# Kernel optimization log

Hardware: AMD Instinct MI355X
Metric: run time of the kernel (lower is better)

Reference implementation:

```python
import jax, jax.numpy as jnp
import numpy as np
import math

B, QL, KL, D = 8, 2048, 2048, 1024


def setup_inputs() -> dict:
    key = jax.random.key(0)
    ks = jax.random.split(key, 9)
    s = 1.0 / math.sqrt(D)
    return {
        "q_embd": jax.random.normal(ks[0], (B, QL, D), jnp.float32),
        "k_embd": jax.random.normal(ks[1], (B, KL, D), jnp.float32),
        "v_embd": jax.random.normal(ks[2], (B, KL, D), jnp.float32),
        "Wq": jax.random.normal(ks[3], (D, D), jnp.float32) * s,
        "bq": jax.random.normal(ks[4], (D,), jnp.float32) * s,
        "Wk": jax.random.normal(ks[5], (D, D), jnp.float32) * s,
        "bk": jax.random.normal(ks[6], (D,), jnp.float32) * s,
        "Wv": jax.random.normal(ks[7], (D, D), jnp.float32) * s,
        "bv": jax.random.normal(ks[8], (D,), jnp.float32) * s,
    }


def reference(q_embd, k_embd, v_embd, Wq, bq, Wk, bk, Wv, bv):
    # Linear projections (torch Linear: x @ W^T + b); head_size==1 so
    # the permute/view multi-head reshuffle is an identity.
    q = jnp.einsum("bsd,hd->bsh", q_embd, Wq) + bq  # [B,QL,D]
    k = jnp.einsum("bsd,hd->bsh", k_embd, Wk) + bk  # [B,KL,D]
    v = jnp.einsum("bsd,hd->bsh", v_embd, Wv) + bv  # [B,KL,D]
    # scaled_dot score: [B,QL,KL]
    scale = 1.0 / jnp.sqrt(jnp.asarray(q.shape[-1], q.dtype))
    score = jnp.einsum("bqd,bkd->bqk", q, k) * scale
    attn = jax.nn.softmax(score, axis=-1)
    out = jnp.einsum("bqk,bkd->bqd", attn, v)  # [B,QL,D]
    return out
```

## Files before the change

kernel.cpp:

```cpp
#include <hip/hip_runtime.h>
#include <hip/hip_bf16.h>

typedef float f32x4 __attribute__((ext_vector_type(4)));
typedef __bf16 bf16x8 __attribute__((ext_vector_type(8)));
typedef unsigned short u16x4 __attribute__((ext_vector_type(4)));

__device__ __forceinline__ unsigned short f2bf(float f) {
  unsigned u = __builtin_bit_cast(unsigned, f);
  u += 0x7FFFu + ((u >> 16) & 1u);
  return (unsigned short)(u >> 16);
}
__device__ __forceinline__ float bf2f(unsigned short h) {
  unsigned u = ((unsigned)h) << 16;
  return __builtin_bit_cast(float, u);
}

__device__ __forceinline__ void gload_lds16(const void* g, void* l) {
  __builtin_amdgcn_global_load_lds(
      (const __attribute__((address_space(1))) void*)g,
      (__attribute__((address_space(3))) void*)l, 16, 0, 0);
}

constexpr int BM = 256, BN = 256, BK = 64;

#define BAR() __builtin_amdgcn_s_barrier()
#define VMW(N) asm volatile("s_waitcnt vmcnt(" #N ")" ::: "memory")
#define PRIO(x) __builtin_amdgcn_s_setprio(x)

#define MM(a_, b_, c_)                                                        \
  c_ = __builtin_amdgcn_mfma_f32_16x16x32_bf16(                               \
      __builtin_bit_cast(bf16x8, a_), __builtin_bit_cast(bf16x8, b_), c_, 0, 0, 0)

template <int OUT_MODE, bool HAS_BIAS>
__global__ __launch_bounds__(512, 2) void gemm256(
    const unsigned short* __restrict__ A, const unsigned short* __restrict__ B,
    const float* __restrict__ bias, float scale, void* __restrict__ Cv,
    int N, int K, long sA, long sB, long sC, const float* __restrict__ rsum,
    int gx, int gy) {
  __shared__ char sm[131072];

  const int nwg = gridDim.x;
  int id = blockIdx.x;
  id = (id & 7) * (nwg >> 3) + (id >> 3);
  const int bx = id % gx;
  const int by = (id / gx) % gy;
  const int bz = id / (gx * gy);

  const int t = threadIdx.x;
  const int lane = t & 63;
  const int w = t >> 6;
  const int wm = w >> 2;
  const int wn = w & 3;

  const int rowBase = by * BM;
  const int colBase = bx * BN;
  const unsigned short* Ab = A + sA * bz;
  const unsigned short* Bb = B + sB * bz;
  const int NT = K >> 6;

  const int srl = lane >> 3;
  const int schunk = (lane & 7) ^ srl;

#define STAGE_A(tt, h, d)                                                     \
  do {                                                                        \
    int _kt = (tt); if (_kt > NT - 1) _kt = NT - 1;                           \
    const int _k0 = _kt << 6;                                                 \
    _Pragma("unroll") for (int _j = 0; _j < 2; ++_j) {                        \
      const int _r = (w + 8 * _j) * 8 + srl;                                  \
      gload_lds16(Ab + (size_t)(rowBase + (h) * 128 + _r) * K + _k0 + schunk * 8, \
                  sm + (d) * 32768 + (h) * 16384 + (w + 8 * _j) * 1024);      \
    }                                                                         \
  } while (0)
#define STAGE_B(tt, h, d)                                                     \
  do {                                                                        \
    int _kt = (tt); if (_kt > NT - 1) _kt = NT - 1;                           \
    const int _k0 = _kt << 6;                                                 \
    _Pragma("unroll") for (int _j = 0; _j < 2; ++_j) {                        \
      const int _r = (w + 8 * _j) * 8 + srl;                                  \
      gload_lds16(Bb + (size_t)(colBase + (h) * 128 + _r) * K + _k0 + schunk * 8, \
                  sm + 65536 + (d) * 32768 + (h) * 16384 + (w + 8 * _j) * 1024); \
    }                                                                         \
  } while (0)

  const int lr = lane & 15;
  const int g0 = lane >> 4;
  const int sw0 = (g0 ^ (lr & 7)) << 4;
  const int sw1 = ((g0 + 4) ^ (lr & 7)) << 4;
  const int aBase = wm * 8192 + lr * 128;
  const int bBase = 65536 + wn * 4096 + lr * 128;

  uint4 Ar[4][2], Br0[2][2], Br1[2][2];
  f32x4 acc[8][4];
#pragma unroll
  for (int m = 0; m < 8; ++m)
#pragma unroll
    for (int n = 0; n < 4; ++n) acc[m][n] = (f32x4){0.f, 0.f, 0.f, 0.f};

#define READ_A(d, mh)                                                         \
  do {                                                                        \
    _Pragma("unroll") for (int f = 0; f < 4; ++f) {                           \
      Ar[f][0] = *(const uint4*)(sm + (d) * 32768 + (mh) * 16384 + aBase + f * 2048 + sw0); \
      Ar[f][1] = *(const uint4*)(sm + (d) * 32768 + (mh) * 16384 + aBase + f * 2048 + sw1); \
    }                                                                         \
  } while (0)
#define READ_B0(d)                                                            \
  do {                                                                        \
    _Pragma("unroll") for (int f = 0; f < 2; ++f) {                           \
      Br0[f][0] = *(const uint4*)(sm + (d) * 32768 + bBase + f * 2048 + sw0); \
      Br0[f][1] = *(const uint4*)(sm + (d) * 32768 + bBase + f * 2048 + sw1); \
    }                                                                         \
  } while (0)
#define READ_B1(d)                                                            \
  do {                                                                        \
    _Pragma("unroll") for (int f = 0; f < 2; ++f) {                           \
      Br1[f][0] = *(const uint4*)(sm + (d) * 32768 + 16384 + bBase + f * 2048 + sw0); \
      Br1[f][1] = *(const uint4*)(sm + (d) * 32768 + 16384 + bBase + f * 2048 + sw1); \
    }                                                                         \
  } while (0)

#define MFMA_Q(Bset, mh, nh)                                                  \
  do {                                                                        \
    _Pragma("unroll") for (int kk = 0; kk < 2; ++kk)                          \
        _Pragma("unroll") for (int mf = 0; mf < 4; ++mf)                      \
            _Pragma("unroll") for (int nf = 0; nf < 2; ++nf)                  \
                MM(Ar[mf][kk], Bset[nf][kk], acc[(mh) * 4 + mf][(nh) * 2 + nf]); \
  } while (0)

#define TILE2(t_, d_)                                                         \
  do {                                                                        \
     READ_B0(d_); READ_B1(d_); READ_A(d_, 0);                       \
    STAGE_A((t_) + 1, 1, (d_) ^ 1);                                           \
    BAR();                                                                    \
    PRIO(1); MFMA_Q(Br0, 0, 0); MFMA_Q(Br1, 0, 1); PRIO(0);                   \
    BAR();                                                                    \
     READ_A(d_, 1);                                                 \
    STAGE_A((t_) + 2, 0, d_); STAGE_B((t_) + 2, 0, d_); STAGE_B((t_) + 2, 1, d_); \
    BAR();                                                                    \
    PRIO(1); MFMA_Q(Br1, 1, 1); MFMA_Q(Br0, 1, 0); PRIO(0);                   \
    VMW(6);                                                                   \
    BAR();                                                                    \
  } while (0)

  STAGE_A(0, 0, 0); STAGE_B(0, 0, 0); STAGE_B(0, 1, 0); STAGE_A(0, 1, 0);
  STAGE_A(1, 0, 1); STAGE_B(1, 0, 1); STAGE_B(1, 1, 1);
  VMW(6);
  BAR();

  for (int i = 0; i < (NT >> 1); ++i) {
    TILE2(2 * i, 0);
    TILE2(2 * i + 1, 1);
  }
  VMW(0);

#pragma unroll
  for (int n = 0; n < 4; ++n) {
    const int col = colBase + (n >> 1) * 128 + wn * 32 + (n & 1) * 16 + lr;
    float bvv = 0.f;
    if constexpr (HAS_BIAS) bvv = bias[col];
#pragma unroll
    for (int m = 0; m < 8; ++m) {
      const int row0 = rowBase + (m >> 2) * 128 + wm * 64 + (m & 3) * 16 + g0 * 4;
      f32x4 v = acc[m][n];
      if constexpr (OUT_MODE == 0) {
        unsigned short* C = (unsigned short*)Cv + sC * bz;
#pragma unroll
        for (int r = 0; r < 4; ++r)
          C[(size_t)(row0 + r) * N + col] = f2bf(v[r] * scale + bvv);
      } else if constexpr (OUT_MODE == 1) {
        unsigned short* C = (unsigned short*)Cv;
        const int b = row0 >> 11, s = row0 & 2047;
        u16x4 pk;
#pragma unroll
        for (int r = 0; r < 4; ++r) pk[r] = f2bf(v[r] * scale + bvv);
        *(u16x4*)&C[((size_t)b * N + col) * 2048 + s] = pk;
      } else if constexpr (OUT_MODE == 2) {
        float* C = (float*)Cv + sC * bz;
        const float4 lv = *(const float4*)&rsum[(size_t)bz * 2048 + row0];
        C[(size_t)(row0 + 0) * N + col] = v[0] / lv.x;
        C[(size_t)(row0 + 1) * N + col] = v[1] / lv.y;
        C[(size_t)(row0 + 2) * N + col] = v[2] / lv.z;
        C[(size_t)(row0 + 3) * N + col] = v[3] / lv.w;
      } else {
        unsigned short* C = (unsigned short*)Cv + sC * bz;
#pragma unroll
        for (int r = 0; r < 4; ++r)
          C[(size_t)(row0 + r) * N + col] = f2bf(__expf(v[r] * scale));
      }
    }
  }
}

__global__ __launch_bounds__(256) void conv_pair(
    const float* __restrict__ e, const float* __restrict__ wt,
    unsigned short* __restrict__ eo, unsigned short* __restrict__ wo,
    int ne8, int nw8) {
  const int tot = ne8 + nw8;
  const int stride = gridDim.x * 256;
  for (int i = blockIdx.x * 256 + threadIdx.x; i < tot; i += stride) {
    const float* src;
    unsigned short* dst;
    int k;
    if (i < ne8) { src = e; dst = eo; k = i; }
    else { src = wt; dst = wo; k = i - ne8; }
    float4 a = ((const float4*)src)[2 * k];
    float4 b = ((const float4*)src)[2 * k + 1];
    unsigned short h[8];
    h[0] = f2bf(a.x); h[1] = f2bf(a.y); h[2] = f2bf(a.z); h[3] = f2bf(a.w);
    h[4] = f2bf(b.x); h[5] = f2bf(b.y); h[6] = f2bf(b.z); h[7] = f2bf(b.w);
    ((uint4*)dst)[k] = *(uint4*)h;
  }
}

__global__ __launch_bounds__(256) void rowsum_kernel(
    const unsigned short* __restrict__ E, float* __restrict__ out) {
  const size_t row = blockIdx.x;
  const unsigned short* p = E + row * 2048;
  const int t = threadIdx.x;
  const int lane = t & 63, wid = t >> 6;

  uint4 x = ((const uint4*)p)[t];
  const unsigned short* hs = (const unsigned short*)&x;
  float s = 0.f;
#pragma unroll
  for (int j = 0; j < 8; ++j) s += bf2f(hs[j]);
#pragma unroll
  for (int d = 1; d < 64; d <<= 1) s += __shfl_xor(s, d);
  __shared__ float red[4];
  if (lane == 0) red[wid] = s;
  __syncthreads();
  if (t == 0) out[row] = red[0] + red[1] + red[2] + red[3];
}

extern "C" void kernel_launch(void* const* d_in, const int* in_sizes, int n_in,
                              void* d_out, int out_size, void* d_ws, size_t ws_size,
                              hipStream_t stream) {
  const float* q_embd = (const float*)d_in[0];
  const float* k_embd = (const float*)d_in[1];
  const float* v_embd = (const float*)d_in[2];
  const float* Wq = (const float*)d_in[3];
  const float* bq = (const float*)d_in[4];
  const float* Wk = (const float*)d_in[5];
  const float* bk = (const float*)d_in[6];
  const float* Wv = (const float*)d_in[7];
  const float* bv = (const float*)d_in[8];

  constexpr int B = 8, QL = 2048, KL = 2048, D = 1024;
  constexpr size_t NE = (size_t)B * QL * D;

  unsigned short* qb = (unsigned short*)d_ws;
  unsigned short* kb = qb + NE;
  unsigned short* vT = kb + NE;
  unsigned short* Sb = vT + NE;
  unsigned short* Xe = Sb;
  unsigned short* Wb = Sb + NE;
  float* rsum = (float*)qb;

  dim3 blk256(256), blk512(512);
  const dim3 gconv(2048);
  const dim3 gproj(4 * 64);
  constexpr int NE8 = (int)(NE / 8), NW8 = D * D / 8;

  conv_pair<<<gconv, blk256, 0, stream>>>(q_embd, Wq, Xe, Wb, NE8, NW8);
  gemm256<0, true><<<gproj, blk512, 0, stream>>>(Xe, Wb, bq, 1.0f, qb, D, D,
                                                 0L, 0L, 0L, nullptr, 4, 64);
  conv_pair<<<gconv, blk256, 0, stream>>>(k_embd, Wk, Xe, Wb, NE8, NW8);
  gemm256<0, true><<<gproj, blk512, 0, stream>>>(Xe, Wb, bk, 1.0f, kb, D, D,
                                                 0L, 0L, 0L, nullptr, 4, 64);
  conv_pair<<<gconv, blk256, 0, stream>>>(v_embd, Wv, Xe, Wb, NE8, NW8);
  gemm256<1, true><<<gproj, blk512, 0, stream>>>(Xe, Wb, bv, 1.0f, vT, D, D,
                                                 0L, 0L, 0L, nullptr, 4, 64);

  gemm256<3, false><<<dim3(512), blk512, 0, stream>>>(
      qb, kb, nullptr, 0.03125f, Sb, KL, D, (long)QL * D, (long)KL * D,
      (long)QL * KL, nullptr, 8, 8);

  rowsum_kernel<<<dim3(B * QL), blk256, 0, stream>>>(Sb, rsum);

  gemm256<2, false><<<dim3(256), blk512, 0, stream>>>(
      Sb, vT, nullptr, 1.0f, d_out, D, KL, (long)QL * KL, (long)D * KL,
      (long)QL * D, rsum, 4, 8);
}
```

Measured before the change: 357.9 us.

## Split each K-tile into four MFMA quadrants interleaved with LDS reads and staging

```diff
diff --git a/kernel.cpp b/kernel.cpp
--- a/kernel.cpp
+++ b/kernel.cpp
@@ -24,6 +24,12 @@
 constexpr int BM = 256, BN = 256, BK = 64;
 
 #define BAR() __builtin_amdgcn_s_barrier()
+#define LGKM0()                                        \
+  do {                                                 \
+    asm volatile("s_waitcnt lgkmcnt(0)" ::: "memory"); \
+    __builtin_amdgcn_sched_barrier(0);                 \
+  } while (0)
+#define LGKM8() asm volatile("s_waitcnt lgkmcnt(8)" ::: "memory")
 #define VMW(N) asm volatile("s_waitcnt vmcnt(" #N ")" ::: "memory")
 #define PRIO(x) __builtin_amdgcn_s_setprio(x)
 
@@ -126,29 +132,43 @@
                 MM(Ar[mf][kk], Bset[nf][kk], acc[(mh) * 4 + mf][(nh) * 2 + nf]); \
   } while (0)
 
-#define TILE2(t_, d_)                                                         \
-  do {                                                                        \
-     READ_B0(d_); READ_B1(d_); READ_A(d_, 0);                       \
+#define TILE4(t_, d_)                                                         \
+  do {                                                                        \
+                           \
+    READ_B0(d_); READ_A(d_, 0);                                               \
     STAGE_A((t_) + 1, 1, (d_) ^ 1);                                           \
-    BAR();                                                                    \
-    PRIO(1); MFMA_Q(Br0, 0, 0); MFMA_Q(Br1, 0, 1); PRIO(0);                   \
-    BAR();                                                                    \
-     READ_A(d_, 1);                                                 \
-    STAGE_A((t_) + 2, 0, d_); STAGE_B((t_) + 2, 0, d_); STAGE_B((t_) + 2, 1, d_); \
-    BAR();                                                                    \
-    PRIO(1); MFMA_Q(Br1, 1, 1); MFMA_Q(Br0, 1, 0); PRIO(0);                   \
+    LGKM8();                                                                  \
+    BAR(); LGKM0();                                                           \
+    PRIO(1); MFMA_Q(Br0, 0, 0); PRIO(0);                                      \
+    BAR();                                                                    \
+             \
+    READ_B1(d_);                                                              \
+    STAGE_B((t_) + 2, 0, d_);                                                 \
+    BAR(); LGKM0();                                                           \
+    PRIO(1); MFMA_Q(Br1, 0, 1); PRIO(0);                                      \
+    BAR();                                                                    \
+             \
+    READ_A(d_, 1);                                                            \
+    STAGE_B((t_) + 2, 1, d_);                                                 \
+    BAR(); LGKM0();                                                           \
+    PRIO(1); MFMA_Q(Br1, 1, 1); PRIO(0);                                      \
+    BAR();                                                                    \
+        \
+    STAGE_A((t_) + 2, 0, d_);                                                 \
+    BAR();                                                                    \
+    PRIO(1); MFMA_Q(Br0, 1, 0); PRIO(0);                                      \
     VMW(6);                                                                   \
     BAR();                                                                    \
   } while (0)
 
-  STAGE_A(0, 0, 0); STAGE_B(0, 0, 0); STAGE_B(0, 1, 0); STAGE_A(0, 1, 0);
-  STAGE_A(1, 0, 1); STAGE_B(1, 0, 1); STAGE_B(1, 1, 1);
+  STAGE_A(0, 0, 0); STAGE_A(0, 1, 0); STAGE_B(0, 0, 0); STAGE_B(0, 1, 0);
+  STAGE_B(1, 0, 1); STAGE_B(1, 1, 1); STAGE_A(1, 0, 1);
   VMW(6);
   BAR();
 
   for (int i = 0; i < (NT >> 1); ++i) {
-    TILE2(2 * i, 0);
-    TILE2(2 * i + 1, 1);
+    TILE4(2 * i, 0);
+    TILE4(2 * i + 1, 1);
   }
   VMW(0);
 
```

New measurement: 381.5 us. 6.6% more time.

## Fuse softmax row-sum into exp-score GEMM epilogue via per-tile partial sums

Applied to the files above, without the earlier changes.

```diff
diff --git a/kernel.cpp b/kernel.cpp
--- a/kernel.cpp
+++ b/kernel.cpp
@@ -31,11 +31,11 @@
   c_ = __builtin_amdgcn_mfma_f32_16x16x32_bf16(                               \
       __builtin_bit_cast(bf16x8, a_), __builtin_bit_cast(bf16x8, b_), c_, 0, 0, 0)
 
-template <int OUT_MODE, bool HAS_BIAS>
+template <int OUT_MODE, bool HAS_BIAS, bool FUSED>
 __global__ __launch_bounds__(512, 2) void gemm256(
     const unsigned short* __restrict__ A, const unsigned short* __restrict__ B,
     const float* __restrict__ bias, float scale, void* __restrict__ Cv,
-    int N, int K, long sA, long sB, long sC, const float* __restrict__ rsum,
+    int N, int K, long sA, long sB, long sC, float* __restrict__ rsum,
     int gx, int gy) {
   __shared__ char sm[131072];
 
@@ -152,39 +152,109 @@
   }
   VMW(0);
 
-#pragma unroll
-  for (int n = 0; n < 4; ++n) {
-    const int col = colBase + (n >> 1) * 128 + wn * 32 + (n & 1) * 16 + lr;
-    float bvv = 0.f;
-    if constexpr (HAS_BIAS) bvv = bias[col];
+  if constexpr (OUT_MODE == 3 && FUSED) {
+    __syncthreads();
+    float* smf = (float*)sm;
+    unsigned short* C = (unsigned short*)Cv + sC * bz;
 #pragma unroll
     for (int m = 0; m < 8; ++m) {
       const int row0 = rowBase + (m >> 2) * 128 + wm * 64 + (m & 3) * 16 + g0 * 4;
-      f32x4 v = acc[m][n];
-      if constexpr (OUT_MODE == 0) {
-        unsigned short* C = (unsigned short*)Cv + sC * bz;
-#pragma unroll
-        for (int r = 0; r < 4; ++r)
-          C[(size_t)(row0 + r) * N + col] = f2bf(v[r] * scale + bvv);
-      } else if constexpr (OUT_MODE == 1) {
-        unsigned short* C = (unsigned short*)Cv;
-        const int b = row0 >> 11, s = row0 & 2047;
-        u16x4 pk;
-#pragma unroll
-        for (int r = 0; r < 4; ++r) pk[r] = f2bf(v[r] * scale + bvv);
-        *(u16x4*)&C[((size_t)b * N + col) * 2048 + s] = pk;
-      } else if constexpr (OUT_MODE == 2) {
-        float* C = (float*)Cv + sC * bz;
-        const float4 lv = *(const float4*)&rsum[(size_t)bz * 2048 + row0];
-        C[(size_t)(row0 + 0) * N + col] = v[0] / lv.x;
-        C[(size_t)(row0 + 1) * N + col] = v[1] / lv.y;
-        C[(size_t)(row0 + 2) * N + col] = v[2] / lv.z;
-        C[(size_t)(row0 + 3) * N + col] = v[3] / lv.w;
-      } else {
-        unsigned short* C = (unsigned short*)Cv + sC * bz;
+      f32x4 rs = (f32x4){0.f, 0.f, 0.f, 0.f};
+#pragma unroll
+      for (int n = 0; n < 4; ++n) {
+        const int col = colBase + (n >> 1) * 128 + wn * 32 + (n & 1) * 16 + lr;
+        f32x4 v = acc[m][n];
+#pragma unroll
+        for (int r = 0; r < 4; ++r) {
+          const unsigned short h = f2bf(__expf(v[r] * scale));
+          C[(size_t)(row0 + r) * N + col] = h;
+          rs[r] += bf2f(h);
+        }
+      }
+#pragma unroll
+      for (int mk = 1; mk < 16; mk <<= 1) {
+        rs[0] += __shfl_xor(rs[0], mk);
+        rs[1] += __shfl_xor(rs[1], mk);
+        rs[2] += __shfl_xor(rs[2], mk);
+        rs[3] += __shfl_xor(rs[3], mk);
+      }
+      if (lr == 0) {
+        const int lrow = row0 - rowBase;
+#pragma unroll
+        for (int r = 0; r < 4; ++r) smf[wn * 256 + lrow + r] = rs[r];
+      }
+    }
+    __syncthreads();
+    if (t < 256) {
+      const float s4 = smf[t] + smf[256 + t] + smf[512 + t] + smf[768 + t];
+      rsum[((size_t)bz * 2048 + rowBase + t) * 8 + bx] = s4;
+    }
+  } else if constexpr (OUT_MODE == 3) {
+    unsigned short* C = (unsigned short*)Cv + sC * bz;
+#pragma unroll
+    for (int n = 0; n < 4; ++n) {
+      const int col = colBase + (n >> 1) * 128 + wn * 32 + (n & 1) * 16 + lr;
+#pragma unroll
+      for (int m = 0; m < 8; ++m) {
+        const int row0 = rowBase + (m >> 2) * 128 + wm * 64 + (m & 3) * 16 + g0 * 4;
+        f32x4 v = acc[m][n];
 #pragma unroll
         for (int r = 0; r < 4; ++r)
           C[(size_t)(row0 + r) * N + col] = f2bf(__expf(v[r] * scale));
+      }
+    }
+  } else if constexpr (OUT_MODE == 2) {
+    float* C = (float*)Cv + sC * bz;
+#pragma unroll
+    for (int m = 0; m < 8; ++m) {
+      const int row0 = rowBase + (m >> 2) * 128 + wm * 64 + (m & 3) * 16 + g0 * 4;
+      f32x4 inv;
+      if constexpr (FUSED) {
+#pragma unroll
+        for (int r = 0; r < 4; ++r) {
+          const size_t pb = ((size_t)bz * 2048 + row0 + r) * 8;
+          const float4 p0 = *(const float4*)&rsum[pb];
+          const float4 p1 = *(const float4*)&rsum[pb + 4];
+          inv[r] = 1.f / (((p0.x + p0.y) + (p0.z + p0.w)) +
+                          ((p1.x + p1.y) + (p1.z + p1.w)));
+        }
+      } else {
+        const float4 lv = *(const float4*)&rsum[(size_t)bz * 2048 + row0];
+        inv[0] = 1.f / lv.x; inv[1] = 1.f / lv.y;
+        inv[2] = 1.f / lv.z; inv[3] = 1.f / lv.w;
+      }
+#pragma unroll
+      for (int n = 0; n < 4; ++n) {
+        const int col = colBase + (n >> 1) * 128 + wn * 32 + (n & 1) * 16 + lr;
+        f32x4 v = acc[m][n];
+#pragma unroll
+        for (int r = 0; r < 4; ++r)
+          C[(size_t)(row0 + r) * N + col] = v[r] * inv[r];
+      }
+    }
+  } else {
+#pragma unroll
+    for (int n = 0; n < 4; ++n) {
+      const int col = colBase + (n >> 1) * 128 + wn * 32 + (n & 1) * 16 + lr;
+      float bvv = 0.f;
+      if constexpr (HAS_BIAS) bvv = bias[col];
+#pragma unroll
+      for (int m = 0; m < 8; ++m) {
+        const int row0 = rowBase + (m >> 2) * 128 + wm * 64 + (m & 3) * 16 + g0 * 4;
+        f32x4 v = acc[m][n];
+        if constexpr (OUT_MODE == 0) {
+          unsigned short* C = (unsigned short*)Cv + sC * bz;
+#pragma unroll
+          for (int r = 0; r < 4; ++r)
+            C[(size_t)(row0 + r) * N + col] = f2bf(v[r] * scale + bvv);
+        } else {
+          unsigned short* C = (unsigned short*)Cv;
+          const int b = row0 >> 11, s = row0 & 2047;
+          u16x4 pk;
+#pragma unroll
+          for (int r = 0; r < 4; ++r) pk[r] = f2bf(v[r] * scale + bvv);
+          *(u16x4*)&C[((size_t)b * N + col) * 2048 + s] = pk;
+        }
       }
     }
   }
@@ -246,6 +316,8 @@
 
   constexpr int B = 8, QL = 2048, KL = 2048, D = 1024;
   constexpr size_t NE = (size_t)B * QL * D;
+  constexpr size_t LAYOUT_BYTES = 3 * NE * 2 + (size_t)B * QL * KL * 2;
+  constexpr size_t PARTIAL_BYTES = (size_t)B * QL * 8 * 4;
 
   unsigned short* qb = (unsigned short*)d_ws;
   unsigned short* kb = qb + NE;
@@ -253,7 +325,9 @@
   unsigned short* Sb = vT + NE;
   unsigned short* Xe = Sb;
   unsigned short* Wb = Sb + NE;
-  float* rsum = (float*)qb;
+
+  const bool fused = ws_size >= LAYOUT_BYTES + PARTIAL_BYTES;
+  float* partial = fused ? (float*)((char*)d_ws + LAYOUT_BYTES) : (float*)qb;
 
   dim3 blk256(256), blk512(512);
   const dim3 gconv(2048);
@@ -261,22 +335,33 @@
   constexpr int NE8 = (int)(NE / 8), NW8 = D * D / 8;
 
   conv_pair<<<gconv, blk256, 0, stream>>>(q_embd, Wq, Xe, Wb, NE8, NW8);
-  gemm256<0, true><<<gproj, blk512, 0, stream>>>(Xe, Wb, bq, 1.0f, qb, D, D,
-                                                 0L, 0L, 0L, nullptr, 4, 64);
+  gemm256<0, true, false><<<gproj, blk512, 0, stream>>>(
+      Xe, Wb, bq, 1.0f, qb, D, D, 0L, 0L, 0L, nullptr, 4, 64);
   conv_pair<<<gconv, blk256, 0, stream>>>(k_embd, Wk, Xe, Wb, NE8, NW8);
-  gemm256<0, true><<<gproj, blk512, 0, stream>>>(Xe, Wb, bk, 1.0f, kb, D, D,
-                                                 0L, 0L, 0L, nullptr, 4, 64);
+  gemm256<0, true, false><<<gproj, blk512, 0, stream>>>(
+      Xe, Wb, bk, 1.0f, kb, D, D, 0L, 0L, 0L, nullptr, 4, 64);
   conv_pair<<<gconv, blk256, 0, stream>>>(v_embd, Wv, Xe, Wb, NE8, NW8);
-  gemm256<1, true><<<gproj, blk512, 0, stream>>>(Xe, Wb, bv, 1.0f, vT, D, D,
-                                                 0L, 0L, 0L, nullptr, 4, 64);
-
-  gemm256<3, false><<<dim3(512), blk512, 0, stream>>>(
-      qb, kb, nullptr, 0.03125f, Sb, KL, D, (long)QL * D, (long)KL * D,
-      (long)QL * KL, nullptr, 8, 8);
-
-  rowsum_kernel<<<dim3(B * QL), blk256, 0, stream>>>(Sb, rsum);
-
-  gemm256<2, false><<<dim3(256), blk512, 0, stream>>>(
-      Sb, vT, nullptr, 1.0f, d_out, D, KL, (long)QL * KL, (long)D * KL,
-      (long)QL * D, rsum, 4, 8);
-}
+  gemm256<1, true, false><<<gproj, blk512, 0, stream>>>(
+      Xe, Wb, bv, 1.0f, vT, D, D, 0L, 0L, 0L, nullptr, 4, 64);
+
+  if (fused) {
+    gemm256<3, false, true><<<dim3(512), blk512, 0, stream>>>(
+        qb, kb, nullptr, 0.03125f, Sb, KL, D, (long)QL * D, (long)KL * D,
+        (long)QL * KL, partial, 8, 8);
+  } else {
+    gemm256<3, false, false><<<dim3(512), blk512, 0, stream>>>(
+        qb, kb, nullptr, 0.03125f, Sb, KL, D, (long)QL * D, (long)KL * D,
+        (long)QL * KL, nullptr, 8, 8);
+    rowsum_kernel<<<dim3(B * QL), blk256, 0, stream>>>(Sb, partial);
+  }
+
+  if (fused) {
+    gemm256<2, false, true><<<dim3(256), blk512, 0, stream>>>(
+        Sb, vT, nullptr, 1.0f, d_out, D, KL, (long)QL * KL, (long)D * KL,
+        (long)QL * D, partial, 4, 8);
+  } else {
+    gemm256<2, false, false><<<dim3(256), blk512, 0, stream>>>(
+        Sb, vT, nullptr, 1.0f, d_out, D, KL, (long)QL * KL, (long)D * KL,
+        (long)QL * D, partial, 4, 8);
+  }
+}
```

Result: faster. 344.5 us (-3.7%).
